# Performance work log

Hardware: AMD Instinct MI355X
Metric: run time of the kernel (lower is better)

## Reference

```python
import jax, jax.numpy as jnp
import numpy as np

N_OBJ = 8        # objects per sample -> nc2 = 28 pair-nodes per sample (code caps nc2 < 30)
MAX_REL = 10     # relations per sample (num_rel is uniform so total_rels is static)


def setup_inputs() -> dict:
    key = jax.random.key(0)
    k1, k2, k3, k4, k5 = jax.random.split(key, 5)
    B, D, n = 1024, 512, N_OBJ
    iu, ju = np.triu_indices(n, k=1)                     # (i<j) pair layout, lexicographic
    nc2 = iu.shape[0]                                     # 28
    bcol = np.repeat(np.arange(B), nc2)
    slicing_tensor = jnp.asarray(
        np.stack([bcol, np.tile(iu, B), np.tile(ju, B)], axis=1), dtype=jnp.int32)  # [B*nc2, 3]
    spatial_branch_feature_map = jax.random.normal(k1, (B * nc2, D), dtype=jnp.float32)
    W_self = jax.random.normal(k2, (D, D), dtype=jnp.float32) / np.float32(np.sqrt(D))
    W_nbr = jax.random.normal(k3, (D, D), dtype=jnp.float32) / np.float32(np.sqrt(D))
    b = jnp.zeros((D,), dtype=jnp.float32)
    # object_pairs: distinct indices in [0, n)
    i0 = jax.random.randint(k4, (B, MAX_REL), 0, n)
    off = jax.random.randint(k5, (B, MAX_REL), 1, n)
    i1 = (i0 + off) % n
    object_pairs = jnp.stack([i0, i1], axis=-1).astype(jnp.int32)  # [B, MAX_REL, 2]
    num_rel = jnp.full((B,), MAX_REL, dtype=jnp.int32)
    num_obj = jnp.full((B,), n, dtype=jnp.int32)
    return {"spatial_branch_feature_map": spatial_branch_feature_map, "W_self": W_self,
            "W_nbr": W_nbr, "b": b, "slicing_tensor": slicing_tensor,
            "object_pairs": object_pairs, "num_rel": num_rel, "num_obj": num_obj}


def reference(spatial_branch_feature_map, W_self, W_nbr, b,
              slicing_tensor, object_pairs, num_rel, num_obj):
    x = spatial_branch_feature_map
    N, D = x.shape
    B = num_obj.shape[0]
    nc2 = N // B                                          # pair-nodes per sample
    n = N_OBJ
    # --- fully-connected edge index per sample (incl. self-loops), offset per batch ---
    src_l = jnp.repeat(jnp.arange(nc2, dtype=jnp.int32), nc2)   # row0: t1 outer loop
    dst_l = jnp.tile(jnp.arange(nc2, dtype=jnp.int32), nc2)     # row1: t2 inner loop
    offs = (jnp.arange(B, dtype=jnp.int32) * nc2)[:, None]
    src = (src_l[None, :] + offs).reshape(-1)                   # [B*nc2^2]
    dst = (dst_l[None, :] + offs).reshape(-1)
    # --- GNN layer: sum-aggregate neighbor messages, linear + ReLU ---
    agg = jax.ops.segment_sum(x[src], dst, num_segments=N)      # [N, D]
    h = jax.nn.relu(x @ W_self + agg @ W_nbr + b)               # [N, D]
    # --- key-matching gather (replaces nested python-loop boolean matching) ---
    keys = slicing_tensor[:, 0] * (n * n) + slicing_tensor[:, 1] * n + slicing_tensor[:, 2]
    lut = jnp.zeros((B * n * n,), dtype=jnp.int32).at[keys].set(jnp.arange(N, dtype=jnp.int32))
    pmin = jnp.minimum(object_pairs[..., 0], object_pairs[..., 1])
    pmax = jnp.maximum(object_pairs[..., 0], object_pairs[..., 1])
    bidx = jnp.arange(B, dtype=jnp.int32)[:, None]
    rel_keys = (bidx * (n * n) + pmin * n + pmax).reshape(-1)   # [B*MAX_REL]
    rows = lut[rel_keys]
    return h[rows]                                              # [total_rels, D]
```

## Files before the change

### kernel.cpp

```cpp
#include <hip/hip_runtime.h>
#include <hip/hip_bf16.h>
#include <stdint.h>


typedef __bf16 bf16_t;
typedef __bf16 bf16x8 __attribute__((ext_vector_type(8)));
typedef __bf16 bf16x4 __attribute__((ext_vector_type(4)));
typedef float  f32x4  __attribute__((ext_vector_type(4)));

#define D_DIM 512
#define NC2   28
#define NOBJ  8
#define MAXREL 10
#define B_SAMP 1024
#define OUTROWS (B_SAMP * MAXREL)

__device__ __forceinline__ void gload_lds16(const void* g, void* l) {
  __builtin_amdgcn_global_load_lds(
      (const __attribute__((address_space(1))) unsigned int*)g,
      (__attribute__((address_space(3))) unsigned int*)l, 16, 0, 0);
}

__global__ __launch_bounds__(256) void prep_kernel(
    const float* __restrict__ x, const float* __restrict__ Wself,
    const float* __restrict__ Wnbr, const int* __restrict__ pairs,
    bf16_t* __restrict__ Sbf, bf16_t* __restrict__ Abf,
    bf16_t* __restrict__ Wst, bf16_t* __restrict__ Wnt)
{
  const int blk = blockIdx.x, tid = threadIdx.x;
  if (blk < B_SAMP) {
    __shared__ int rel_row[MAXREL];
    __shared__ float4 oddsum[128];
    if (tid < MAXREL) {
      int p0 = pairs[blk * MAXREL * 2 + tid * 2 + 0];
      int p1 = pairs[blk * MAXREL * 2 + tid * 2 + 1];
      int pmin = min(p0, p1), pmax = max(p0, p1);
      rel_row[tid] = 7 * pmin - (pmin * (pmin - 1)) / 2 + (pmax - pmin - 1);
    }
    __syncthreads();
    int rr[MAXREL];
    #pragma unroll
    for (int j = 0; j < MAXREL; ++j) rr[j] = rel_row[j];

    const int h = tid >> 7, c = tid & 127;
    const float4* x4 = (const float4*)(x + (size_t)blk * NC2 * D_DIM);
    float4 a = {0.f, 0.f, 0.f, 0.f};
    #pragma unroll
    for (int rp = 0; rp < NC2 / 2; ++rp) {
      int r = rp * 2 + h;
      float4 v = x4[r * 128 + c];
      a.x += v.x; a.y += v.y; a.z += v.z; a.w += v.w;
      bf16x4 o = { (bf16_t)v.x, (bf16_t)v.y, (bf16_t)v.z, (bf16_t)v.w };
      #pragma unroll
      for (int j = 0; j < MAXREL; ++j)
        if (rr[j] == r)
          *(bf16x4*)(Abf + (size_t)(blk * MAXREL + j) * D_DIM + c * 4) = o;
    }
    if (h) oddsum[c] = a;
    __syncthreads();
    if (!h) {
      float4 b = oddsum[c];
      bf16x4 o = { (bf16_t)(a.x + b.x), (bf16_t)(a.y + b.y),
                   (bf16_t)(a.z + b.z), (bf16_t)(a.w + b.w) };
      *(bf16x4*)(Sbf + (size_t)blk * D_DIM + c * 4) = o;
    }
  } else {
    __shared__ float tile[32][33];
    const int t = blk - B_SAMP;
    const float* W  = (t & 256) ? Wnbr : Wself;
    bf16_t*     Wt  = (t & 256) ? Wnt  : Wst;
    const int r = t & 255;
    const int k0 = (r & 15) * 32, n0 = (r >> 4) * 32;
    const int tx = tid & 31, ty = tid >> 5;
    #pragma unroll
    for (int i = 0; i < 32; i += 8)
      tile[ty + i][tx] = W[(size_t)(k0 + ty + i) * D_DIM + n0 + tx];
    __syncthreads();
    #pragma unroll
    for (int i = 0; i < 32; i += 8)
      Wt[(size_t)(n0 + ty + i) * D_DIM + k0 + tx] = (bf16_t)tile[tx][ty + i];
  }
}

#define SA_BYTES 6144
#define SB_BYTES 8192
__global__ __launch_bounds__(256) void fused_gemm_kernel(
    const bf16_t* __restrict__ Abf, const bf16_t* __restrict__ Sbf,
    const bf16_t* __restrict__ Wst, const bf16_t* __restrict__ Wnt,
    const float* __restrict__ bias, float* __restrict__ out)
{
  __shared__ __align__(16) unsigned char pool[2 * SA_BYTES + 2 * SB_BYTES];

  const int tid = threadIdx.x;
  const int w = tid >> 6, l = tid & 63;
  const int kg = l >> 4, lr = l & 15;
  const int n0 = blockIdx.y * 64;
  const int n0w = n0 + w * 16;
  const int arow0 = blockIdx.x * 80;
  const int srow0 = blockIdx.x * 8;

  f32x4 acc[6] = {};

  auto STAGE = [&](int bsel, int k0) {
    bf16_t* aB = (bf16_t*)(pool + bsel * SA_BYTES);
    bf16_t* bB = (bf16_t*)(pool + 2 * SA_BYTES + bsel * SB_BYTES);
    #pragma unroll
    for (int r = 0; r < 4; ++r) {
      int slot = r * 4 + w;
      if (slot < 6) {
        int c = slot * 64 + l;
        int row = c >> 2, ch = c & 3;
        int sch = ch ^ ((row >> 1) & 3);
        const bf16_t* g = (slot < 5)
            ? Abf + (size_t)(arow0 + row) * D_DIM + k0 + sch * 8
            : Sbf + (size_t)(srow0 + (row & 7)) * D_DIM + k0 + sch * 8;
        gload_lds16(g, aB + (size_t)slot * 512);
      } else if (slot < 14) {
        int c = (slot - 6) * 64 + l;
        int mat = c >> 8, rc = c & 255;
        int row = rc >> 2, ch = rc & 3;
        int sch = ch ^ ((row >> 1) & 3);
        const bf16_t* W = mat ? Wnt : Wst;
        gload_lds16(W + (size_t)(n0 + row) * D_DIM + k0 + sch * 8,
                    bB + (size_t)(slot - 6) * 512);
      }
    }
  };

  STAGE(0, 0);
  __syncthreads();

  const int xorc = (kg ^ ((lr >> 1) & 3)) * 8;
  int cur = 0;
  #pragma unroll 2
  for (int t = 0; t < 16; ++t) {
    if (t < 15) STAGE(cur ^ 1, (t + 1) * 32);

    const bf16_t* aC = (const bf16_t*)(pool + cur * SA_BYTES);
    const bf16_t* bC = (const bf16_t*)(pool + 2 * SA_BYTES + cur * SB_BYTES);
    bf16x8 af[6], bs, bn;
    #pragma unroll
    for (int s = 0; s < 6; ++s)
      af[s] = *(const bf16x8*)(aC + (s * 16 + lr) * 32 + xorc);
    bs = *(const bf16x8*)(bC + (w * 16 + lr) * 32 + xorc);
    bn = *(const bf16x8*)(bC + 2048 + (w * 16 + lr) * 32 + xorc);

    #pragma unroll
    for (int s = 0; s < 5; ++s)
      acc[s] = __builtin_amdgcn_mfma_f32_16x16x32_bf16(af[s], bs, acc[s], 0, 0, 0);
    acc[5] = __builtin_amdgcn_mfma_f32_16x16x32_bf16(af[5], bn, acc[5], 0, 0, 0);

    __syncthreads();
    cur ^= 1;
  }

  float* Tex = (float*)pool;
  #pragma unroll
  for (int reg = 0; reg < 4; ++reg)
    Tex[(w * 8 + ((kg * 4 + reg) & 7)) * 20 + lr] = acc[5][reg];
  __syncthreads();

  const float bv = bias[n0w + lr];
  #pragma unroll
  for (int s = 0; s < 5; ++s) {
    #pragma unroll
    for (int reg = 0; reg < 4; ++reg) {
      int rloc = s * 16 + kg * 4 + reg;
      int ls = rloc / MAXREL;
      float v = acc[s][reg] + Tex[(w * 8 + ls) * 20 + lr] + bv;
      out[(size_t)(arow0 + rloc) * D_DIM + n0w + lr] = fmaxf(v, 0.0f);
    }
  }
}

extern "C" void kernel_launch(void* const* d_in, const int* in_sizes, int n_in,
                              void* d_out, int out_size, void* d_ws, size_t ws_size,
                              hipStream_t stream) {
  const float* x     = (const float*)d_in[0];
  const float* Wself = (const float*)d_in[1];
  const float* Wnbr  = (const float*)d_in[2];
  const float* bias  = (const float*)d_in[3];
  const int*   pairs = (const int*)d_in[5];

  char* ws = (char*)d_ws;
  size_t off = 0;
  bf16_t* Sbf = (bf16_t*)(ws + off); off += (size_t)B_SAMP * D_DIM * 2;
  bf16_t* Wst = (bf16_t*)(ws + off); off += (size_t)D_DIM * D_DIM * 2;
  bf16_t* Wnt = (bf16_t*)(ws + off); off += (size_t)D_DIM * D_DIM * 2;
  bf16_t* Abf = (bf16_t*)(ws + off); off += (size_t)OUTROWS * D_DIM * 2;

  prep_kernel<<<B_SAMP + 512, 256, 0, stream>>>(
      x, Wself, Wnbr, pairs, Sbf, Abf, Wst, Wnt);
  fused_gemm_kernel<<<dim3(OUTROWS / 80, D_DIM / 64), 256, 0, stream>>>(
      Abf, Sbf, Wst, Wnt, bias, (float*)d_out);
}
```

Baseline: 35.08 us.

## Gather relation rows from fp32 x directly inside GEMM instead of staging Abf

The prep kernel no longer writes a bf16 copy of the gathered relation rows (Abf). The GEMM now computes the row indices from object_pairs and loads fp32 x rows, converting them to bf16 in registers before storing them into swizzled LDS. This removes a global write and re-read of about 10 MB. In exchange, the A-tile loads become synchronous register loads of twice the bytes, repeated across all 8 column blocks, instead of async global_load_lds.

```diff
diff --git a/kernel.cpp b/kernel.cpp
--- a/kernel.cpp
+++ b/kernel.cpp
@@ -23,38 +23,19 @@
 
 __global__ __launch_bounds__(256) void prep_kernel(
     const float* __restrict__ x, const float* __restrict__ Wself,
-    const float* __restrict__ Wnbr, const int* __restrict__ pairs,
-    bf16_t* __restrict__ Sbf, bf16_t* __restrict__ Abf,
-    bf16_t* __restrict__ Wst, bf16_t* __restrict__ Wnt)
+    const float* __restrict__ Wnbr,
+    bf16_t* __restrict__ Sbf, bf16_t* __restrict__ Wst, bf16_t* __restrict__ Wnt)
 {
   const int blk = blockIdx.x, tid = threadIdx.x;
   if (blk < B_SAMP) {
-    __shared__ int rel_row[MAXREL];
     __shared__ float4 oddsum[128];
-    if (tid < MAXREL) {
-      int p0 = pairs[blk * MAXREL * 2 + tid * 2 + 0];
-      int p1 = pairs[blk * MAXREL * 2 + tid * 2 + 1];
-      int pmin = min(p0, p1), pmax = max(p0, p1);
-      rel_row[tid] = 7 * pmin - (pmin * (pmin - 1)) / 2 + (pmax - pmin - 1);
-    }
-    __syncthreads();
-    int rr[MAXREL];
-    #pragma unroll
-    for (int j = 0; j < MAXREL; ++j) rr[j] = rel_row[j];
-
     const int h = tid >> 7, c = tid & 127;
     const float4* x4 = (const float4*)(x + (size_t)blk * NC2 * D_DIM);
     float4 a = {0.f, 0.f, 0.f, 0.f};
     #pragma unroll
     for (int rp = 0; rp < NC2 / 2; ++rp) {
-      int r = rp * 2 + h;
-      float4 v = x4[r * 128 + c];
+      float4 v = x4[(rp * 2 + h) * 128 + c];
       a.x += v.x; a.y += v.y; a.z += v.z; a.w += v.w;
-      bf16x4 o = { (bf16_t)v.x, (bf16_t)v.y, (bf16_t)v.z, (bf16_t)v.w };
-      #pragma unroll
-      for (int j = 0; j < MAXREL; ++j)
-        if (rr[j] == r)
-          *(bf16x4*)(Abf + (size_t)(blk * MAXREL + j) * D_DIM + c * 4) = o;
     }
     if (h) oddsum[c] = a;
     __syncthreads();
@@ -85,11 +66,13 @@
 #define SA_BYTES 6144
 #define SB_BYTES 8192
 __global__ __launch_bounds__(256) void fused_gemm_kernel(
-    const bf16_t* __restrict__ Abf, const bf16_t* __restrict__ Sbf,
+    const float* __restrict__ x, const bf16_t* __restrict__ Sbf,
     const bf16_t* __restrict__ Wst, const bf16_t* __restrict__ Wnt,
-    const float* __restrict__ bias, float* __restrict__ out)
+    const int* __restrict__ pairs, const float* __restrict__ bias,
+    float* __restrict__ out)
 {
   __shared__ __align__(16) unsigned char pool[2 * SA_BYTES + 2 * SB_BYTES];
+  __shared__ int xrow[80];
 
   const int tid = threadIdx.x;
   const int w = tid >> 6, l = tid & 63;
@@ -99,31 +82,44 @@
   const int arow0 = blockIdx.x * 80;
   const int srow0 = blockIdx.x * 8;
 
+  if (tid < 80) {
+    int sm = srow0 + tid / MAXREL, j = tid % MAXREL;
+    int p0 = pairs[(size_t)(sm * MAXREL + j) * 2 + 0];
+    int p1 = pairs[(size_t)(sm * MAXREL + j) * 2 + 1];
+    int pmin = min(p0, p1), pmax = max(p0, p1);
+    xrow[tid] = sm * NC2 + 7 * pmin - (pmin * (pmin - 1)) / 2 + (pmax - pmin - 1);
+  }
+  __syncthreads();
+
   f32x4 acc[6] = {};
 
   auto STAGE = [&](int bsel, int k0) {
     bf16_t* aB = (bf16_t*)(pool + bsel * SA_BYTES);
     bf16_t* bB = (bf16_t*)(pool + 2 * SA_BYTES + bsel * SB_BYTES);
     #pragma unroll
-    for (int r = 0; r < 4; ++r) {
-      int slot = r * 4 + w;
-      if (slot < 6) {
-        int c = slot * 64 + l;
-        int row = c >> 2, ch = c & 3;
-        int sch = ch ^ ((row >> 1) & 3);
-        const bf16_t* g = (slot < 5)
-            ? Abf + (size_t)(arow0 + row) * D_DIM + k0 + sch * 8
-            : Sbf + (size_t)(srow0 + (row & 7)) * D_DIM + k0 + sch * 8;
-        gload_lds16(g, aB + (size_t)slot * 512);
-      } else if (slot < 14) {
-        int c = (slot - 6) * 64 + l;
-        int mat = c >> 8, rc = c & 255;
-        int row = rc >> 2, ch = rc & 3;
-        int sch = ch ^ ((row >> 1) & 3);
-        const bf16_t* W = mat ? Wnt : Wst;
-        gload_lds16(W + (size_t)(n0 + row) * D_DIM + k0 + sch * 8,
-                    bB + (size_t)(slot - 6) * 512);
+    for (int r = 0; r < 2; ++r) {
+      int bslot = r * 4 + w;
+      int c = bslot * 64 + l;
+      int mat = c >> 8, rc = c & 255;
+      int row = rc >> 2, ch = rc & 3;
+      int sch = ch ^ ((row >> 1) & 3);
+      const bf16_t* W = mat ? Wnt : Wst;
+      gload_lds16(W + (size_t)(n0 + row) * D_DIM + k0 + sch * 8,
+                  bB + (size_t)c * 8);
+    }
+    #pragma unroll
+    for (int r = 0; r < 3; ++r) {
+      int idx = r * 256 + tid;
+      int row = idx >> 3, kq = idx & 7;
+      int slot8 = (((kq >> 1) ^ ((row >> 1) & 3)) << 1) + (kq & 1);
+      bf16x4 val;
+      if (row < 80) {
+        float4 v = *(const float4*)(x + (size_t)xrow[row] * D_DIM + k0 + kq * 4);
+        val = bf16x4{ (bf16_t)v.x, (bf16_t)v.y, (bf16_t)v.z, (bf16_t)v.w };
+      } else {
+        val = *(const bf16x4*)(Sbf + (size_t)(srow0 + (row & 7)) * D_DIM + k0 + kq * 4);
       }
+      *(bf16x4*)(aB + row * 32 + slot8 * 4) = val;
     }
   };
 
@@ -187,10 +183,8 @@
   bf16_t* Sbf = (bf16_t*)(ws + off); off += (size_t)B_SAMP * D_DIM * 2;
   bf16_t* Wst = (bf16_t*)(ws + off); off += (size_t)D_DIM * D_DIM * 2;
   bf16_t* Wnt = (bf16_t*)(ws + off); off += (size_t)D_DIM * D_DIM * 2;
-  bf16_t* Abf = (bf16_t*)(ws + off); off += (size_t)OUTROWS * D_DIM * 2;
 
-  prep_kernel<<<B_SAMP + 512, 256, 0, stream>>>(
-      x, Wself, Wnbr, pairs, Sbf, Abf, Wst, Wnt);
+  prep_kernel<<<B_SAMP + 512, 256, 0, stream>>>(x, Wself, Wnbr, Sbf, Wst, Wnt);
   fused_gemm_kernel<<<dim3(OUTROWS / 80, D_DIM / 64), 256, 0, stream>>>(
-      Abf, Sbf, Wst, Wnt, bias, (float*)d_out);
+      x, Sbf, Wst, Wnt, pairs, bias, (float*)d_out);
 }
```

Result: slower. 45.40 us (+29.4%).
